# Kernel optimization log

Measured on AMD Instinct MI355X. Metric: run time of the kernel, lower is better.

The kernel has to match this reference:

```python
import jax, jax.numpy as jnp
import numpy as np

NUM_GROUPS = 32
NUM_HEADS = 8  # channels=512 / num_head_channels=64
EPS = 1e-5


def group_norm(x, gamma, beta):
    # x: [B, C, T]
    b, c, t = x.shape
    xg = x.reshape(b, NUM_GROUPS, (c // NUM_GROUPS) * t)
    mean = xg.mean(axis=-1, keepdims=True)
    var = xg.var(axis=-1, keepdims=True)
    xg = (xg - mean) * jax.lax.rsqrt(var + EPS)
    return xg.reshape(b, c, t) * gamma[None, :, None] + beta[None, :, None]


def setup_inputs() -> dict:
    key = jax.random.key(0)
    ks = jax.random.split(key, 8)
    B, C, H, W = 16, 512, 32, 32
    E = 1024
    x = jax.random.normal(ks[0], (B, C, H, W), dtype=jnp.float32)
    emb = jax.random.normal(ks[1], (B, E), dtype=jnp.float32)
    gn_gamma = jnp.ones((C,), jnp.float32)
    gn_beta = jnp.zeros((C,), jnp.float32)
    # FiLM: Linear(emb_channels, 2*channels), weight init std=0.001, bias zero
    emb_w = jax.random.normal(ks[2], (2 * C, E), dtype=jnp.float32) * 0.001
    emb_b = jnp.zeros((2 * C,), jnp.float32)
    # conv1x1 qkv: [3C, C]
    qkv_w = jax.random.normal(ks[3], (3 * C, C), dtype=jnp.float32) * (1.0 / np.sqrt(C))
    qkv_b = jnp.zeros((3 * C,), jnp.float32)
    # proj_out conv1x1 (zero-init in original; use small random so grads flow)
    proj_w = jax.random.normal(ks[4], (C, C), dtype=jnp.float32) * 0.02
    proj_b = jnp.zeros((C,), jnp.float32)
    return dict(x=x, emb=emb, gn_gamma=gn_gamma, gn_beta=gn_beta,
                emb_w=emb_w, emb_b=emb_b, qkv_w=qkv_w, qkv_b=qkv_b,
                proj_w=proj_w, proj_b=proj_b)


def reference(x, emb, gn_gamma, gn_beta, emb_w, emb_b, qkv_w, qkv_b, proj_w, proj_b):
    b, c, h_sp, w_sp = x.shape
    t = h_sp * w_sp
    xr = x.reshape(b, c, t)
    h = group_norm(xr, gn_gamma, gn_beta)
    # FiLM conditioning
    e = jax.nn.silu(emb) @ emb_w.T + emb_b  # [B, 2C]
    scale, shift = jnp.split(e, 2, axis=1)
    h = h * (1.0 + scale[:, :, None]) + shift[:, :, None]
    # conv1x1 QKV
    qkv = jnp.einsum('oc,bct->bot', qkv_w, h) + qkv_b[None, :, None]  # [B, 3C, T]
    ch = c // NUM_HEADS
    qkv = qkv.reshape(b * NUM_HEADS, 3 * ch, t)  # legacy head ordering
    q, k, v = jnp.split(qkv, 3, axis=1)
    s = 1.0 / jnp.sqrt(jnp.sqrt(jnp.float32(ch)))
    w = jnp.einsum('bct,bcs->bts', q * s, k * s)  # [B*H, T, T]
    w = jax.nn.softmax(w, axis=-1)
    a = jnp.einsum('bts,bcs->bct', w, v).reshape(b, c, t)
    out = jnp.einsum('oc,bct->bot', proj_w, a) + proj_b[None, :, None]
    return (xr + out).reshape(b, c, h_sp, w_sp)
```

## Files before the change

### kernel.cpp

```cpp
#include <hip/hip_runtime.h>
#include <hip/hip_bf16.h>

typedef __hip_bfloat16 bf16;
typedef __attribute__((ext_vector_type(8))) short short8;
typedef __attribute__((ext_vector_type(4))) float f32x4;
typedef __attribute__((ext_vector_type(4))) unsigned short us4;
typedef __attribute__((ext_vector_type(2))) unsigned short us2;

#define B_  16
#define C_  512
#define T_  1024
#define G_  32
#define CPG 16
#define E_  1024
#define NH  8
#define CH  64
#define CT  (C_ * T_)

__device__ __forceinline__ float b2f(bf16 v) { return __bfloat162float(v); }
__device__ __forceinline__ unsigned short fbits_fast(float v) {
  unsigned int u = __builtin_bit_cast(unsigned int, v);
  u += 0x7fff + ((u >> 16) & 1);
  return (unsigned short)(u >> 16);
}
__device__ __forceinline__ bf16 f2b_fast(float v) {
  unsigned short s = fbits_fast(v);
  return *reinterpret_cast<bf16*>(&s);
}
__device__ __forceinline__ unsigned int cvtpk(float lo, float hi) {
  unsigned int r;
  asm("v_cvt_pk_bf16_f32 %0, %1, %2" : "=v"(r) : "v"(lo), "v"(hi));
  return r;
}

__device__ __forceinline__ void gload16(const void* g, void* l) {
  __builtin_amdgcn_global_load_lds(
      (const __attribute__((address_space(1))) void*)g,
      (__attribute__((address_space(3))) void*)l, 16, 0, 0);
}

__global__ __launch_bounds__(256) void convert_w_kernel(
    const float* __restrict__ qkv_w, const float* __restrict__ proj_w,
    bf16* __restrict__ wq, bf16* __restrict__ wp) {
  int i4 = blockIdx.x * 256 + threadIdx.x;
  const int NQ4 = (3 * C_ * C_) / 4;
  const float* src;
  unsigned short* dst;
  int off;
  if (i4 < NQ4) {
    src = qkv_w; dst = (unsigned short*)wq; off = i4;
  } else {
    src = proj_w; dst = (unsigned short*)wp; off = i4 - NQ4;
  }
  float4 v = *(const float4*)(src + (size_t)off * 4);
  uint2 pk = {cvtpk(v.x, v.y), cvtpk(v.z, v.w)};
  *(uint2*)(dst + (size_t)off * 4) = pk;
}

__global__ __launch_bounds__(256) void convert_one(
    const float* __restrict__ src, bf16* __restrict__ dst) {
  int i4 = blockIdx.x * 256 + threadIdx.x;
  float4 v = *(const float4*)(src + (size_t)i4 * 4);
  uint2 pk = {cvtpk(v.x, v.y), cvtpk(v.z, v.w)};
  *(uint2*)((unsigned short*)dst + (size_t)i4 * 4) = pk;
}

__global__ __launch_bounds__(256) void film2_kernel(
    const float* __restrict__ emb, const float* __restrict__ emb_w,
    const float* __restrict__ emb_b, float* __restrict__ e_out) {
  __shared__ float S[B_ * E_];
  int tid = threadIdx.x;
  float4* S4 = (float4*)S;
  const float4* e4 = (const float4*)emb;
  for (int i = tid; i < (B_ * E_) / 4; i += 256) {
    float4 v = e4[i];
    float4 o;
    o.x = v.x / (1.f + __expf(-v.x));
    o.y = v.y / (1.f + __expf(-v.y));
    o.z = v.z / (1.f + __expf(-v.z));
    o.w = v.w / (1.f + __expf(-v.w));
    S4[i] = o;
  }
  __syncthreads();
  int wave = tid >> 6, lane = tid & 63;
  int j = blockIdx.x * 4 + wave;
  const float4* w4p = (const float4*)(emb_w + (size_t)j * E_);
  float4 w4[4];
#pragma unroll
  for (int k = 0; k < 4; k++) w4[k] = w4p[k * 64 + lane];
  float bias = emb_b[j];
  for (int b = 0; b < B_; b++) {
    const float4* Sb = (const float4*)(S + b * E_);
    float acc = 0.f;
#pragma unroll
    for (int k = 0; k < 4; k++) {
      float4 s = Sb[k * 64 + lane];
      acc += w4[k].x * s.x + w4[k].y * s.y + w4[k].z * s.z + w4[k].w * s.w;
    }
#pragma unroll
    for (int off = 1; off < 64; off <<= 1) acc += __shfl_xor(acc, off, 64);
    if (lane == 0) e_out[b * (2 * C_) + j] = acc + bias;
  }
}

__global__ __launch_bounds__(1024) void gn_stats_kernel(
    const float* __restrict__ x, float* __restrict__ mean_buf,
    float* __restrict__ rstd_buf) {
  int bg = blockIdx.x;
  const float4* b4 = (const float4*)(x + (size_t)bg * (CPG * T_));
  int tid = threadIdx.x;
  float s = 0.f, sq = 0.f;
#pragma unroll
  for (int p = 0; p < 4; p++) {
    float4 v = b4[p * 1024 + tid];
    s += v.x + v.y + v.z + v.w;
    sq += v.x * v.x + v.y * v.y + v.z * v.z + v.w * v.w;
  }
  for (int off = 32; off > 0; off >>= 1) {
    s += __shfl_down(s, off, 64);
    sq += __shfl_down(sq, off, 64);
  }
  __shared__ float ss[16], ssq[16];
  int wid = tid >> 6, lane = tid & 63;
  if (lane == 0) { ss[wid] = s; ssq[wid] = sq; }
  __syncthreads();
  if (tid == 0) {
    float S = 0.f, Q = 0.f;
#pragma unroll
    for (int w = 0; w < 16; w++) { S += ss[w]; Q += ssq[w]; }
    const float inv_n = 1.f / (CPG * T_);
    float m = S * inv_n;
    float var = Q * inv_n - m * m;
    mean_buf[bg] = m;
    rstd_buf[bg] = rsqrtf(fmaxf(var, 0.f) + 1e-5f);
  }
}

__global__ __launch_bounds__(256) void norm_film_t2(
    const float* __restrict__ x, const float* __restrict__ mean_buf,
    const float* __restrict__ rstd_buf, const float* __restrict__ gamma,
    const float* __restrict__ beta, const float* __restrict__ e_buf,
    bf16* __restrict__ h, int b0) {
  __shared__ unsigned short S[64][66];
  __shared__ float pm[64], pr[64], pa[64];
  int t0 = blockIdx.x * 64;
  int c0 = blockIdx.y * 64;
  int bl = blockIdx.z;
  int b = b0 + bl;
  int tid = threadIdx.x;
  if (tid < 64) {
    int c = c0 + tid;
    int g = c >> 4;
    float m = mean_buf[b * G_ + g];
    float r = rstd_buf[b * G_ + g];
    float sc = 1.f + e_buf[b * 2 * C_ + c];
    float sh = e_buf[b * 2 * C_ + C_ + c];
    pm[tid] = m;
    pr[tid] = r * gamma[c] * sc;
    pa[tid] = beta[c] * sc + sh;
  }
  __syncthreads();
  const float* xb = x + ((size_t)b * C_ + c0) * T_ + t0;
#pragma unroll
  for (int p = 0; p < 4; p++) {
    int i = p * 256 + tid;
    int cl = i >> 4, t4 = (i & 15) * 4;
    float4 v = *(const float4*)(xb + (size_t)cl * T_ + t4);
    float m = pm[cl], r = pr[cl], ad = pa[cl];
    *(unsigned int*)&S[cl][t4] = cvtpk((v.x - m) * r + ad, (v.y - m) * r + ad);
    *(unsigned int*)&S[cl][t4 + 2] =
        cvtpk((v.z - m) * r + ad, (v.w - m) * r + ad);
  }
  __syncthreads();
  unsigned short* hg = (unsigned short*)h + ((size_t)bl * T_ + t0) * C_ + c0;
#pragma unroll
  for (int p = 0; p < 2; p++) {
    int i = p * 256 + tid;
    int tr = i >> 3, c8 = (i & 7) * 8;
    unsigned int w0 = (unsigned int)S[c8 + 0][tr] |
                      ((unsigned int)S[c8 + 1][tr] << 16);
    unsigned int w1 = (unsigned int)S[c8 + 2][tr] |
                      ((unsigned int)S[c8 + 3][tr] << 16);
    unsigned int w2 = (unsigned int)S[c8 + 4][tr] |
                      ((unsigned int)S[c8 + 5][tr] << 16);
    unsigned int w3 = (unsigned int)S[c8 + 6][tr] |
                      ((unsigned int)S[c8 + 7][tr] << 16);
    int4 pk = {(int)w0, (int)w1, (int)w2, (int)w3};
    *(int4*)(hg + (size_t)tr * C_ + c8) = pk;
  }
}

#define ST_STRIDE 264
__global__ __launch_bounds__(256) void qkv_gemm_mfma4(
    const bf16* __restrict__ h, const bf16* __restrict__ wq,
    const float* __restrict__ qkv_b, bf16* __restrict__ qb,
    bf16* __restrict__ kb, bf16* __restrict__ vb, int ngroups) {
  __shared__ __align__(16) unsigned short LB[20480];
  int bid = blockIdx.x;
  int g, o;
  if ((ngroups & 7) == 0) {
    int xcd = bid & 7, j = bid >> 3;
    o = j % 24;
    int slot = j / 24;
    g = slot * 8 + xcd;
  } else {
    o = bid % 24;
    g = bid / 24;
  }
  int tst = g & 3;
  int bl = g >> 2;
  int o0 = o * 64;
  int tb = tst * 256;
  int tid = threadIdx.x;
  int wave = tid >> 6, lane = tid & 63;
  int col = lane & 15, quad = lane >> 4;
  int cs = col & 7;
  int w64 = wave * 64;
  const unsigned short* hg = (const unsigned short*)h + (size_t)bl * T_ * C_;
  const unsigned short* wg = (const unsigned short*)wq;
  char* lds = (char*)LB;
  f32x4 acc[4][4];
  for (int i = 0; i < 4; i++)
    for (int j2 = 0; j2 < 4; j2++) acc[i][j2] = f32x4{0, 0, 0, 0};
  for (int c0 = 0; c0 < C_; c0 += 64) {
    __syncthreads();
#pragma unroll
    for (int p = 0; p < 8; p++) {
      int i = p * 256 + tid;
      int row = i >> 3;
      int sci = (i & 7) ^ (row & 7);
      gload16(hg + (size_t)(tb + row) * C_ + c0 + sci * 8,
              lds + (p * 256 + wave * 64) * 16);
    }
#pragma unroll
    for (int p = 0; p < 2; p++) {
      int i = p * 256 + tid;
      int row = i >> 3;
      int sci = (i & 7) ^ (row & 7);
      gload16(wg + (size_t)(o0 + row) * C_ + c0 + sci * 8,
              lds + 32768 + (p * 256 + wave * 64) * 16);
    }
    __syncthreads();
#pragma unroll
    for (int ks = 0; ks < 2; ks++) {
      short8 af[4], bfr[4];
#pragma unroll
      for (int mt = 0; mt < 4; mt++)
        af[mt] = *(const short8*)&LB[(w64 + mt * 16 + col) * 64 +
                                     (((ks * 4 + quad) ^ cs) << 3)];
#pragma unroll
      for (int nt = 0; nt < 4; nt++)
        bfr[nt] = *(const short8*)&LB[16384 + (nt * 16 + col) * 64 +
                                      (((ks * 4 + quad) ^ cs) << 3)];
#pragma unroll
      for (int mt = 0; mt < 4; mt++)
#pragma unroll
        for (int nt = 0; nt < 4; nt++)
          acc[mt][nt] = __builtin_amdgcn_mfma_f32_16x16x32_bf16(
              af[mt], bfr[nt], acc[mt][nt], 0, 0, 0);
    }
  }
  int sec = (o0 >> 6) % 3;
  int hd = o0 / 192;
  const float s = 0.35355339059327373f;
  const float sq = s * 1.4426950408889634f;
  if (sec < 2) {
    bf16* dst = (sec == 0) ? qb : kb;
    float sc = (sec == 0) ? sq : s;
    size_t hb = (size_t)(bl * NH + hd) * T_ * CH;
    for (int mt = 0; mt < 4; mt++) {
      for (int r = 0; r < 4; r++) {
        int t = tb + w64 + mt * 16 + quad * 4 + r;
        for (int nt = 0; nt < 4; nt++) {
          int ch = nt * 16 + col;
          dst[hb + (size_t)t * CH + ch] =
              f2b_fast((acc[mt][nt][r] + qkv_b[o0 + ch]) * sc);
        }
      }
    }
  } else {
    __syncthreads();
    for (int mt = 0; mt < 4; mt++) {
      for (int r = 0; r < 4; r++) {
        int tl = w64 + mt * 16 + quad * 4 + r;
        for (int nt = 0; nt < 4; nt++) {
          int ch = nt * 16 + col;
          LB[ch * ST_STRIDE + tl] =
              fbits_fast(acc[mt][nt][r] + qkv_b[o0 + ch]);
        }
      }
    }
    __syncthreads();
    int rr = tid >> 2, csx = (tid & 3) * 64;
    size_t base = ((size_t)(bl * NH + hd) * CH + rr) * T_ + tb + csx;
    unsigned short* vg = (unsigned short*)vb;
    for (int j2 = 0; j2 < 8; j2++)
      *(int4*)(vg + base + j2 * 8) =
          *(const int4*)&LB[rr * ST_STRIDE + csx + j2 * 8];
  }
}

__global__ __launch_bounds__(256, 4) void attn_mfma8(
    const bf16* __restrict__ qb, const bf16* __restrict__ kb,
    const bf16* __restrict__ vb, bf16* __restrict__ a, int nbh) {
  __shared__ __align__(16) unsigned short LB[20480];
  int bid = blockIdx.x;
  int bh = bid % nbh;
  int qt0 = (bid / nbh) * 128;
  int tid = threadIdx.x;
  int wave = tid >> 6, lane = tid & 63;
  int col = lane & 15, quad = lane >> 4;
  int cs = col & 7;
  int ps = (col >> 1) & 3;
  const unsigned short* qg = (const unsigned short*)qb;
  const unsigned short* kg = (const unsigned short*)kb;
  const unsigned short* vg = (const unsigned short*)vb;
  const size_t tmaj = (size_t)bh * T_ * CH;
  const size_t cmaj = (size_t)bh * CH * T_;
  char* lds = (char*)LB;

  int qrow = qt0 + wave * 16 + col;
  short8 bq0[2], bq1[2];
#pragma unroll
  for (int u = 0; u < 2; u++) {
    const unsigned short* qp = qg + tmaj + (size_t)(qrow + u * 64) * CH;
    bq0[u] = *(const short8*)(qp + quad * 8);
    bq1[u] = *(const short8*)(qp + 32 + quad * 8);
  }
  f32x4 Ot0[4], Ot1[4];
#pragma unroll
  for (int mt = 0; mt < 4; mt++) {
    Ot0[mt] = f32x4{0, 0, 0, 0};
    Ot1[mt] = f32x4{0, 0, 0, 0};
  }
  const short ob = (short)0x3F80;
  short8 ones = {ob, ob, ob, ob, ob, ob, ob, ob};
  f32x4 La0 = f32x4{0, 0, 0, 0}, La1 = f32x4{0, 0, 0, 0};
  unsigned short* pw0 = LB + 16384 + wave * 512 + col * 32;
  unsigned short* pw1 = pw0 + 2048;

#define STAGE(buf, tt)                                                        \
  do {                                                                        \
    int s0_ = (tt) * 64;                                                      \
    const unsigned short* kt_ = kg + tmaj + (size_t)s0_ * CH;                 \
    const unsigned short* vt_ = vg + cmaj + s0_;                              \
    _Pragma("unroll") for (int cc = 0; cc < 2; cc++) {                        \
      int i_ = cc * 256 + tid;                                                \
      int row_ = i_ >> 3;                                                     \
      int sci_ = (i_ & 7) ^ (row_ & 7);                                       \
      int wb_ = (cc * 256 + wave * 64) * 16;       \
      gload16(kt_ + (size_t)row_ * CH + sci_ * 8, lds + (buf) * 8192 + wb_);  \
      gload16(vt_ + (size_t)row_ * T_ + sci_ * 8,                             \
              lds + 16384 + (buf) * 8192 + wb_);                              \
    }                                                                         \
  } while (0)

  STAGE(0, 0);
  __syncthreads();
  int cur = 0;
  for (int t = 0; t < 16; t++) {
    if (t < 15) STAGE(cur ^ 1, t + 1);
    const char* ksb = lds + cur * 8192;
    const char* vtb = lds + 16384 + cur * 8192;
    f32x4 St0[4], St1[4];
#pragma unroll
    for (int mt = 0; mt < 4; mt++) {
      St0[mt] = f32x4{0, 0, 0, 0};
      St1[mt] = f32x4{0, 0, 0, 0};
    }
    __builtin_amdgcn_s_setprio(1);
#pragma unroll
    for (int mt = 0; mt < 4; mt++) {
      int rb = (mt * 16 + col) * 128;
      short8 ak0 = *(const short8*)(ksb + rb + ((quad ^ cs) << 4));
      short8 ak1 = *(const short8*)(ksb + rb + (((quad + 4) ^ cs) << 4));
      St0[mt] = __builtin_amdgcn_mfma_f32_16x16x32_bf16(ak0, bq0[0], St0[mt], 0, 0, 0);
      St1[mt] = __builtin_amdgcn_mfma_f32_16x16x32_bf16(ak0, bq0[1], St1[mt], 0, 0, 0);
      St0[mt] = __builtin_amdgcn_mfma_f32_16x16x32_bf16(ak1, bq1[0], St0[mt], 0, 0, 0);
      St1[mt] = __builtin_amdgcn_mfma_f32_16x16x32_bf16(ak1, bq1[1], St1[mt], 0, 0, 0);
    }
    __builtin_amdgcn_s_setprio(0);
#pragma unroll
    for (int mt = 0; mt < 4; mt++)
#pragma unroll
      for (int r = 0; r < 4; r++) {
        St0[mt][r] = __builtin_amdgcn_exp2f(St0[mt][r]);
        St1[mt][r] = __builtin_amdgcn_exp2f(St1[mt][r]);
      }
#pragma unroll
    for (int kc = 0; kc < 2; kc++) {
#pragma unroll
      for (int mh = 0; mh < 2; mh++) {
        int mt = kc * 2 + mh;
        int wsw = (((2 * mh + (quad >> 1)) ^ ps) << 3) + (quad & 1) * 4;
        uint2 k0 = {cvtpk(St0[mt][0], St0[mt][1]),
                    cvtpk(St0[mt][2], St0[mt][3])};
        uint2 k1 = {cvtpk(St1[mt][0], St1[mt][1]),
                    cvtpk(St1[mt][2], St1[mt][3])};
        *(uint2*)(pw0 + wsw) = k0;
        *(uint2*)(pw1 + wsw) = k1;
      }
      int rsw = (quad ^ ps) << 3;
      short8 bp0 = *(const short8*)(pw0 + rsw);
      short8 bp1 = *(const short8*)(pw1 + rsw);
      __builtin_amdgcn_s_setprio(1);
      La0 = __builtin_amdgcn_mfma_f32_16x16x32_bf16(ones, bp0, La0, 0, 0, 0);
      La1 = __builtin_amdgcn_mfma_f32_16x16x32_bf16(ones, bp1, La1, 0, 0, 0);
#pragma unroll
      for (int mt = 0; mt < 4; mt++) {
        short8 av = *(const short8*)(vtb + (mt * 16 + col) * 128 +
                                     (((kc * 4 + quad) ^ cs) << 4));
        Ot0[mt] = __builtin_amdgcn_mfma_f32_16x16x32_bf16(av, bp0, Ot0[mt], 0, 0, 0);
        Ot1[mt] = __builtin_amdgcn_mfma_f32_16x16x32_bf16(av, bp1, Ot1[mt], 0, 0, 0);
      }
      __builtin_amdgcn_s_setprio(0);
    }
    __syncthreads();
    cur ^= 1;
  }
#undef STAGE
  int bl = bh >> 3, hd = bh & 7;
  unsigned short* ag = (unsigned short*)a;
#pragma unroll
  for (int u = 0; u < 2; u++) {
    float inv = 1.f / ((u == 0) ? La0[0] : La1[0]);
    const f32x4* Ou = (u == 0) ? Ot0 : Ot1;
    size_t rowb = ((size_t)bl * T_ + qrow + u * 64) * C_ + hd * CH;
#pragma unroll
    for (int mt = 0; mt < 4; mt++) {
      uint2 pk = {cvtpk(Ou[mt][0] * inv, Ou[mt][1] * inv),
                  cvtpk(Ou[mt][2] * inv, Ou[mt][3] * inv)};
      *(uint2*)(ag + rowb + mt * 16 + quad * 4) = pk;
    }
  }
}

__global__ __launch_bounds__(256) void proj_mfma3(
    const bf16* __restrict__ a, const bf16* __restrict__ wp,
    const float* __restrict__ proj_b, const float* __restrict__ x,
    float* __restrict__ out, int b0) {
  __shared__ __align__(16) unsigned short LB[8192];
  int bl = blockIdx.z;
  int b = b0 + bl;
  int o0 = blockIdx.y * 64;
  int t0 = blockIdx.x * 64;
  int tid = threadIdx.x;
  int wave = tid >> 6, lane = tid & 63;
  int col = lane & 15, quad = lane >> 4;
  int cs = col & 7;
  int m0 = wave * 16;
  const unsigned short* ag = (const unsigned short*)a + (size_t)bl * T_ * C_;
  const unsigned short* wg = (const unsigned short*)wp;
  char* lds = (char*)LB;
  f32x4 acc[4] = {f32x4{0,0,0,0}, f32x4{0,0,0,0}, f32x4{0,0,0,0}, f32x4{0,0,0,0}};
  for (int c0 = 0; c0 < C_; c0 += 64) {
    __syncthreads();
#pragma unroll
    for (int cc = 0; cc < 2; cc++) {
      int i = cc * 256 + tid;
      int row = i >> 3;
      int sci = (i & 7) ^ (row & 7);
      int wb = (cc * 256 + wave * 64) * 16;
      gload16(ag + (size_t)(t0 + row) * C_ + c0 + sci * 8, lds + wb);
      gload16(wg + (size_t)(o0 + row) * C_ + c0 + sci * 8, lds + 8192 + wb);
    }
    __syncthreads();
#pragma unroll
    for (int ks = 0; ks < 2; ks++) {
      short8 aw = *(const short8*)&LB[4096 + (m0 + col) * 64 +
                                      (((ks * 4 + quad) ^ cs) << 3)];
#pragma unroll
      for (int nt = 0; nt < 4; nt++) {
        short8 ba = *(const short8*)&LB[(nt * 16 + col) * 64 +
                                        (((ks * 4 + quad) ^ cs) << 3)];
        acc[nt] = __builtin_amdgcn_mfma_f32_16x16x32_bf16(aw, ba, acc[nt], 0, 0, 0);
      }
    }
  }
  for (int r = 0; r < 4; r++) {
    int o = o0 + m0 + quad * 4 + r;
    float bias = proj_b[o];
    size_t rowb = ((size_t)b * C_ + o) * T_ + t0;
    for (int nt = 0; nt < 4; nt++) {
      int t = nt * 16 + col;
      out[rowb + t] = x[rowb + t] + acc[nt][r] + bias;
    }
  }
}

extern "C" void kernel_launch(void* const* d_in, const int* in_sizes, int n_in,
                              void* d_out, int out_size, void* d_ws,
                              size_t ws_size, hipStream_t stream) {
  const float* x      = (const float*)d_in[0];
  const float* emb    = (const float*)d_in[1];
  const float* gamma  = (const float*)d_in[2];
  const float* beta   = (const float*)d_in[3];
  const float* emb_w  = (const float*)d_in[4];
  const float* emb_b  = (const float*)d_in[5];
  const float* qkv_w  = (const float*)d_in[6];
  const float* qkv_b  = (const float*)d_in[7];
  const float* proj_w = (const float*)d_in[8];
  const float* proj_b = (const float*)d_in[9];
  float* out = (float*)d_out;

  const size_t BUF16 = (size_t)16 * CT * sizeof(bf16);
  const size_t FULL4 = 4 * BUF16;
  const size_t SCR   = 131072 + (size_t)4 * C_ * C_ * sizeof(bf16);

  if (ws_size >= FULL4) {
    bf16* h_buf = (bf16*)d_ws;
    bf16* q_buf = h_buf + BUF16 / sizeof(bf16);
    bf16* k_buf = q_buf + BUF16 / sizeof(bf16);
    bf16* v_buf = k_buf + BUF16 / sizeof(bf16);
    bool inWs = ws_size >= FULL4 + SCR;
    char* scr = inWs ? ((char*)d_ws + FULL4) : (char*)d_out;
    float* e_buf    = (float*)scr;
    float* mean_buf = e_buf + B_ * 2 * C_;
    float* rstd_buf = mean_buf + B_ * G_;
    bf16*  wq_bf    = (bf16*)(scr + 131072);
    bf16*  wp_bf;

    if (inWs) {
      wp_bf = wq_bf + (size_t)3 * C_ * C_;
      convert_w_kernel<<<dim3(1024), 256, 0, stream>>>(qkv_w, proj_w, wq_bf,
                                                       wp_bf);
    } else {
      wp_bf = q_buf;
      convert_one<<<dim3(768), 256, 0, stream>>>(qkv_w, wq_bf);
    }
    film2_kernel<<<dim3(256), 256, 0, stream>>>(emb, emb_w, emb_b, e_buf);
    gn_stats_kernel<<<dim3(B_ * G_), 1024, 0, stream>>>(x, mean_buf, rstd_buf);
    norm_film_t2<<<dim3(16, 8, 16), 256, 0, stream>>>(
        x, mean_buf, rstd_buf, gamma, beta, e_buf, h_buf, 0);
    qkv_gemm_mfma4<<<dim3(24 * 64), 256, 0, stream>>>(h_buf, wq_bf, qkv_b,
                                                      q_buf, k_buf, v_buf, 64);
    attn_mfma8<<<dim3(8 * 128), 256, 0, stream>>>(q_buf, k_buf, v_buf, h_buf,
                                                  128);
    if (!inWs)
      convert_one<<<dim3(256), 256, 0, stream>>>(proj_w, wp_bf);
    proj_mfma3<<<dim3(16, 8, 16), 256, 0, stream>>>(h_buf, wp_bf, proj_b, x,
                                                    out, 0);
  } else {
    float* e_buf    = (float*)d_ws;
    float* mean_buf = e_buf + B_ * 2 * C_;
    float* rstd_buf = mean_buf + B_ * G_;
    bf16*  wq_bf    = (bf16*)((char*)d_ws + 131072);
    bf16*  wp_bf    = wq_bf + (size_t)3 * C_ * C_;
    bf16* pool = (bf16*)((char*)d_ws + SCR);
    size_t avail = ws_size > SCR ? ws_size - SCR : 0;
    int NB = 16;
    while (NB > 1 && (size_t)4 * NB * CT * sizeof(bf16) > avail) NB >>= 1;
    bf16* h_buf = pool;
    bf16* q_buf = h_buf + (size_t)NB * CT;
    bf16* k_buf = q_buf + (size_t)NB * CT;
    bf16* v_buf = k_buf + (size_t)NB * CT;

    convert_w_kernel<<<dim3(1024), 256, 0, stream>>>(qkv_w, proj_w, wq_bf,
                                                     wp_bf);
    film2_kernel<<<dim3(256), 256, 0, stream>>>(emb, emb_w, emb_b, e_buf);
    gn_stats_kernel<<<dim3(B_ * G_), 1024, 0, stream>>>(x, mean_buf, rstd_buf);
    for (int b0 = 0; b0 < B_; b0 += NB) {
      norm_film_t2<<<dim3(16, 8, NB), 256, 0, stream>>>(
          x, mean_buf, rstd_buf, gamma, beta, e_buf, h_buf, b0);
      qkv_gemm_mfma4<<<dim3(24 * 4 * NB), 256, 0, stream>>>(
          h_buf, wq_bf, qkv_b, q_buf, k_buf, v_buf, 4 * NB);
      int nbh = NB * NH;
      attn_mfma8<<<dim3(8 * nbh), 256, 0, stream>>>(q_buf, k_buf, v_buf,
                                                    h_buf, nbh);
      proj_mfma3<<<dim3(16, 8, NB), 256, 0, stream>>>(h_buf, wp_bf, proj_b, x,
                                                      out, b0);
    }
  }
}
```

Measured before the change: 221.5 us.

## Double-buffer LDS tiles in QKV and projection GEMMs to overlap loads with MFMA

Both the QKV GEMM and the output projection GEMM now keep two LDS buffers. Each issues the global-to-LDS loads for the next K slice before computing on the current one, and drops one of the two barriers per iteration. s_setprio is raised around the MFMA section. This is meant to hide global load latency behind matrix compute, at the cost of doubling LDS per block (80 KB for QKV), which may lower occupancy.

```diff
diff --git a/kernel.cpp b/kernel.cpp
--- a/kernel.cpp
+++ b/kernel.cpp
@@ -191,11 +191,11 @@
 }
 
 #define ST_STRIDE 264
-__global__ __launch_bounds__(256) void qkv_gemm_mfma4(
+__global__ __launch_bounds__(256) void qkv_gemm_mfma5(
     const bf16* __restrict__ h, const bf16* __restrict__ wq,
     const float* __restrict__ qkv_b, bf16* __restrict__ qb,
     bf16* __restrict__ kb, bf16* __restrict__ vb, int ngroups) {
-  __shared__ __align__(16) unsigned short LB[20480];
+  __shared__ __align__(16) unsigned short LB[40960];
   int bid = blockIdx.x;
   int g, o;
   if ((ngroups & 7) == 0) {
@@ -222,36 +222,44 @@
   f32x4 acc[4][4];
   for (int i = 0; i < 4; i++)
     for (int j2 = 0; j2 < 4; j2++) acc[i][j2] = f32x4{0, 0, 0, 0};
-  for (int c0 = 0; c0 < C_; c0 += 64) {
-    __syncthreads();
-#pragma unroll
-    for (int p = 0; p < 8; p++) {
-      int i = p * 256 + tid;
-      int row = i >> 3;
-      int sci = (i & 7) ^ (row & 7);
-      gload16(hg + (size_t)(tb + row) * C_ + c0 + sci * 8,
-              lds + (p * 256 + wave * 64) * 16);
-    }
-#pragma unroll
-    for (int p = 0; p < 2; p++) {
-      int i = p * 256 + tid;
-      int row = i >> 3;
-      int sci = (i & 7) ^ (row & 7);
-      gload16(wg + (size_t)(o0 + row) * C_ + c0 + sci * 8,
-              lds + 32768 + (p * 256 + wave * 64) * 16);
-    }
-    __syncthreads();
+
+#define QSTAGE(buf, c0_)                                                      \
+  do {                                                                        \
+    _Pragma("unroll") for (int p = 0; p < 8; p++) {                           \
+      int i_ = p * 256 + tid;                                                 \
+      int row_ = i_ >> 3;                                                     \
+      int sci_ = (i_ & 7) ^ (row_ & 7);                                       \
+      gload16(hg + (size_t)(tb + row_) * C_ + (c0_) + sci_ * 8,               \
+              lds + (buf) * 40960 + (p * 256 + wave * 64) * 16);              \
+    }                                                                         \
+    _Pragma("unroll") for (int p = 0; p < 2; p++) {                           \
+      int i_ = p * 256 + tid;                                                 \
+      int row_ = i_ >> 3;                                                     \
+      int sci_ = (i_ & 7) ^ (row_ & 7);                                       \
+      gload16(wg + (size_t)(o0 + row_) * C_ + (c0_) + sci_ * 8,               \
+              lds + (buf) * 40960 + 32768 + (p * 256 + wave * 64) * 16);      \
+    }                                                                         \
+  } while (0)
+
+  QSTAGE(0, 0);
+  __syncthreads();
+  int cur = 0;
+  for (int kst = 0; kst < 8; kst++) {
+    if (kst < 7) QSTAGE(cur ^ 1, (kst + 1) * 64);
+    const unsigned short* hb = LB + cur * 20480;
+    const unsigned short* wb2 = hb + 16384;
+    __builtin_amdgcn_s_setprio(1);
 #pragma unroll
     for (int ks = 0; ks < 2; ks++) {
       short8 af[4], bfr[4];
 #pragma unroll
       for (int mt = 0; mt < 4; mt++)
-        af[mt] = *(const short8*)&LB[(w64 + mt * 16 + col) * 64 +
+        af[mt] = *(const short8*)&hb[(w64 + mt * 16 + col) * 64 +
                                      (((ks * 4 + quad) ^ cs) << 3)];
 #pragma unroll
       for (int nt = 0; nt < 4; nt++)
-        bfr[nt] = *(const short8*)&LB[16384 + (nt * 16 + col) * 64 +
-                                      (((ks * 4 + quad) ^ cs) << 3)];
+        bfr[nt] = *(const short8*)&wb2[(nt * 16 + col) * 64 +
+                                       (((ks * 4 + quad) ^ cs) << 3)];
 #pragma unroll
       for (int mt = 0; mt < 4; mt++)
 #pragma unroll
@@ -259,7 +267,11 @@
           acc[mt][nt] = __builtin_amdgcn_mfma_f32_16x16x32_bf16(
               af[mt], bfr[nt], acc[mt][nt], 0, 0, 0);
     }
-  }
+    __builtin_amdgcn_s_setprio(0);
+    __syncthreads();
+    cur ^= 1;
+  }
+#undef QSTAGE
   int sec = (o0 >> 6) % 3;
   int hd = o0 / 192;
   const float s = 0.35355339059327373f;
@@ -267,19 +279,18 @@
   if (sec < 2) {
     bf16* dst = (sec == 0) ? qb : kb;
     float sc = (sec == 0) ? sq : s;
-    size_t hb = (size_t)(bl * NH + hd) * T_ * CH;
+    size_t hb2 = (size_t)(bl * NH + hd) * T_ * CH;
     for (int mt = 0; mt < 4; mt++) {
       for (int r = 0; r < 4; r++) {
         int t = tb + w64 + mt * 16 + quad * 4 + r;
         for (int nt = 0; nt < 4; nt++) {
           int ch = nt * 16 + col;
-          dst[hb + (size_t)t * CH + ch] =
+          dst[hb2 + (size_t)t * CH + ch] =
               f2b_fast((acc[mt][nt][r] + qkv_b[o0 + ch]) * sc);
         }
       }
     }
   } else {
-    __syncthreads();
     for (int mt = 0; mt < 4; mt++) {
       for (int r = 0; r < 4; r++) {
         int tl = w64 + mt * 16 + quad * 4 + r;
@@ -435,11 +446,11 @@
   }
 }
 
-__global__ __launch_bounds__(256) void proj_mfma3(
+__global__ __launch_bounds__(256) void proj_mfma4(
     const bf16* __restrict__ a, const bf16* __restrict__ wp,
     const float* __restrict__ proj_b, const float* __restrict__ x,
     float* __restrict__ out, int b0) {
-  __shared__ __align__(16) unsigned short LB[8192];
+  __shared__ __align__(16) unsigned short LB[16384];
   int bl = blockIdx.z;
   int b = b0 + bl;
   int o0 = blockIdx.y * 64;
@@ -453,30 +464,45 @@
   const unsigned short* wg = (const unsigned short*)wp;
   char* lds = (char*)LB;
   f32x4 acc[4] = {f32x4{0,0,0,0}, f32x4{0,0,0,0}, f32x4{0,0,0,0}, f32x4{0,0,0,0}};
-  for (int c0 = 0; c0 < C_; c0 += 64) {
-    __syncthreads();
-#pragma unroll
-    for (int cc = 0; cc < 2; cc++) {
-      int i = cc * 256 + tid;
-      int row = i >> 3;
-      int sci = (i & 7) ^ (row & 7);
-      int wb = (cc * 256 + wave * 64) * 16;
-      gload16(ag + (size_t)(t0 + row) * C_ + c0 + sci * 8, lds + wb);
-      gload16(wg + (size_t)(o0 + row) * C_ + c0 + sci * 8, lds + 8192 + wb);
-    }
-    __syncthreads();
+
+#define PSTAGE(buf, c0_)                                                      \
+  do {                                                                        \
+    _Pragma("unroll") for (int cc = 0; cc < 2; cc++) {                        \
+      int i_ = cc * 256 + tid;                                                \
+      int row_ = i_ >> 3;                                                     \
+      int sci_ = (i_ & 7) ^ (row_ & 7);                                       \
+      int wb_ = (cc * 256 + wave * 64) * 16;                                  \
+      gload16(ag + (size_t)(t0 + row_) * C_ + (c0_) + sci_ * 8,               \
+              lds + (buf) * 16384 + wb_);                                     \
+      gload16(wg + (size_t)(o0 + row_) * C_ + (c0_) + sci_ * 8,               \
+              lds + (buf) * 16384 + 8192 + wb_);                              \
+    }                                                                         \
+  } while (0)
+
+  PSTAGE(0, 0);
+  __syncthreads();
+  int cur = 0;
+  for (int kst = 0; kst < 8; kst++) {
+    if (kst < 7) PSTAGE(cur ^ 1, (kst + 1) * 64);
+    const unsigned short* ab = LB + cur * 8192;
+    const unsigned short* wb2 = ab + 4096;
+    __builtin_amdgcn_s_setprio(1);
 #pragma unroll
     for (int ks = 0; ks < 2; ks++) {
-      short8 aw = *(const short8*)&LB[4096 + (m0 + col) * 64 +
-                                      (((ks * 4 + quad) ^ cs) << 3)];
+      short8 aw = *(const short8*)&wb2[(m0 + col) * 64 +
+                                       (((ks * 4 + quad) ^ cs) << 3)];
 #pragma unroll
       for (int nt = 0; nt < 4; nt++) {
-        short8 ba = *(const short8*)&LB[(nt * 16 + col) * 64 +
+        short8 ba = *(const short8*)&ab[(nt * 16 + col) * 64 +
                                         (((ks * 4 + quad) ^ cs) << 3)];
         acc[nt] = __builtin_amdgcn_mfma_f32_16x16x32_bf16(aw, ba, acc[nt], 0, 0, 0);
       }
     }
-  }
+    __builtin_amdgcn_s_setprio(0);
+    __syncthreads();
+    cur ^= 1;
+  }
+#undef PSTAGE
   for (int r = 0; r < 4; r++) {
     int o = o0 + m0 + quad * 4 + r;
     float bias = proj_b[o];
@@ -532,13 +558,13 @@
     gn_stats_kernel<<<dim3(B_ * G_), 1024, 0, stream>>>(x, mean_buf, rstd_buf);
     norm_film_t2<<<dim3(16, 8, 16), 256, 0, stream>>>(
         x, mean_buf, rstd_buf, gamma, beta, e_buf, h_buf, 0);
-    qkv_gemm_mfma4<<<dim3(24 * 64), 256, 0, stream>>>(h_buf, wq_bf, qkv_b,
+    qkv_gemm_mfma5<<<dim3(24 * 64), 256, 0, stream>>>(h_buf, wq_bf, qkv_b,
                                                       q_buf, k_buf, v_buf, 64);
     attn_mfma8<<<dim3(8 * 128), 256, 0, stream>>>(q_buf, k_buf, v_buf, h_buf,
                                                   128);
     if (!inWs)
       convert_one<<<dim3(256), 256, 0, stream>>>(proj_w, wp_bf);
-    proj_mfma3<<<dim3(16, 8, 16), 256, 0, stream>>>(h_buf, wp_bf, proj_b, x,
+    proj_mfma4<<<dim3(16, 8, 16), 256, 0, stream>>>(h_buf, wp_bf, proj_b, x,
                                                     out, 0);
   } else {
     float* e_buf    = (float*)d_ws;
@@ -562,12 +588,12 @@
     for (int b0 = 0; b0 < B_; b0 += NB) {
       norm_film_t2<<<dim3(16, 8, NB), 256, 0, stream>>>(
           x, mean_buf, rstd_buf, gamma, beta, e_buf, h_buf, b0);
-      qkv_gemm_mfma4<<<dim3(24 * 4 * NB), 256, 0, stream>>>(
+      qkv_gemm_mfma5<<<dim3(24 * 4 * NB), 256, 0, stream>>>(
           h_buf, wq_bf, qkv_b, q_buf, k_buf, v_buf, 4 * NB);
       int nbh = NB * NH;
       attn_mfma8<<<dim3(8 * nbh), 256, 0, stream>>>(q_buf, k_buf, v_buf,
                                                     h_buf, nbh);
-      proj_mfma3<<<dim3(16, 8, NB), 256, 0, stream>>>(h_buf, wp_bf, proj_b, x,
+      proj_mfma4<<<dim3(16, 8, NB), 256, 0, stream>>>(h_buf, wp_bf, proj_b, x,
                                                       out, b0);
     }
   }
```

Result: no change. 223.4 us (+0.8%).
